# Kernel optimization log

Hardware: AMD Instinct MI355X
Metric: run time of the kernel (lower is better)

## Reference

```python
import jax, jax.numpy as jnp
import numpy as np
import math

H = 2048
NH = 16
NKV = 4
HD = H // NH  # 128
N_REP = NH // NKV
EPS = 1e-6


def rms_norm(x, w, eps=1e-6):
    x32 = x.astype(jnp.float32)
    y = x32 * jax.lax.rsqrt(jnp.mean(x32 * x32, axis=-1, keepdims=True) + eps)
    return (y * w.astype(jnp.float32)).astype(x.dtype)


def mha(normed, key_in, val_in, q_w, k_w, v_w, o_w, bias):
    # normed: [b,s,H]; key_in/val_in: [b,n,H]; bias broadcastable to [b,nh,s,n]
    b, s, _ = normed.shape
    n = key_in.shape[1]
    q = (normed @ q_w).reshape(b, s, NH, HD).transpose(0, 2, 1, 3)      # [b,nh,s,d]
    k = (key_in @ k_w).reshape(b, n, NKV, HD).transpose(0, 2, 1, 3)     # [b,nkv,n,d]
    v = (val_in @ v_w).reshape(b, n, NKV, HD).transpose(0, 2, 1, 3)
    k = jnp.repeat(k, N_REP, axis=1)  # GQA expand -> [b,nh,n,d]
    v = jnp.repeat(v, N_REP, axis=1)
    scores = jnp.einsum('bhsd,bhnd->bhsn', q, k) / math.sqrt(HD) + bias
    probs = jax.nn.softmax(scores.astype(jnp.float32), axis=-1).astype(q.dtype)
    out = jnp.einsum('bhsn,bhnd->bhsd', probs, v)
    out = out.transpose(0, 2, 1, 3).reshape(b, s, NH * HD) @ o_w
    return out, probs


def setup_inputs() -> dict:
    key = jax.random.key(0)
    ks = jax.random.split(key, 20)
    B, S, ND, T = 2, 2048, 64, 2048
    w = lambda k, sh: (jax.random.normal(k, sh, dtype=jnp.float32) * 0.02)
    return {
        'hidden_states': jax.random.normal(ks[0], (B, S, H), dtype=jnp.float32),
        'doc_summary_key': jax.random.normal(ks[1], (B, ND, H), dtype=jnp.float32),
        'doc_summary_value': jax.random.normal(ks[2], (B, ND, H), dtype=jnp.float32),
        'doc_summary_mask': jnp.ones((B, ND), dtype=jnp.float32),
        'token_key': jax.random.normal(ks[3], (B, T, H), dtype=jnp.float32),
        'token_value': jax.random.normal(ks[4], (B, T, H), dtype=jnp.float32),
        'token_mask': jnp.ones((B, T), dtype=jnp.float32),
        'cn_w': jnp.ones((H,), dtype=jnp.float32),
        'cq_w': w(ks[5], (H, NH * HD)),
        'ck_w': w(ks[6], (H, NKV * HD)),
        'cv_w': w(ks[7], (H, NKV * HD)),
        'co_w': w(ks[8], (NH * HD, H)),
        'c_gate': jnp.array([-1.0], dtype=jnp.float32),
        'fn_w': jnp.ones((H,), dtype=jnp.float32),
        'fq_w': w(ks[9], (H, NH * HD)),
        'fk_w': w(ks[10], (H, NKV * HD)),
        'fv_w': w(ks[11], (H, NKV * HD)),
        'fo_w': w(ks[12], (NH * HD, H)),
        'f_gate': jnp.array([-1.0], dtype=jnp.float32),
        'doc_token_map': jax.random.randint(ks[13], (B, T), 0, ND, dtype=jnp.int64)
            if jax.config.jax_enable_x64 else jax.random.randint(ks[13], (B, T), 0, ND).astype(jnp.int32),
    }


def reference(hidden_states, doc_summary_key, doc_summary_value, doc_summary_mask,
              token_key, token_value, token_mask,
              cn_w, cq_w, ck_w, cv_w, co_w, c_gate,
              fn_w, fq_w, fk_w, fv_w, fo_w, f_gate,
              doc_token_map):
    # ---- coarse stage: cross-attention over document summaries ----
    normed = rms_norm(hidden_states, cn_w)
    coarse_bias = ((1.0 - doc_summary_mask) * -1e9)[:, None, None, :]  # [b,1,1,nd]
    attn_out, probs = mha(normed, doc_summary_key, doc_summary_value,
                          cq_w, ck_w, cv_w, co_w, coarse_bias)
    doc_scores = probs.mean(axis=(1, 2))  # [b,nd] avg over heads+query positions
    gate_c = jax.nn.sigmoid(c_gate).astype(attn_out.dtype)
    out = hidden_states + gate_c * attn_out

    # ---- fine stage: cross-attention over token KV with log-doc-score bias ----
    log_ds = jnp.log(doc_scores + EPS)
    doc_bias = jnp.take_along_axis(log_ds, doc_token_map, axis=1)  # [b,T]
    pad_bias = (1.0 - token_mask) * -1e9
    fine_bias = (doc_bias + pad_bias)[:, None, None, :]  # [b,1,1,T]
    normed_f = rms_norm(out, fn_w)
    attn_out_f, _ = mha(normed_f, token_key, token_value,
                        fq_w, fk_w, fv_w, fo_w, fine_bias)
    gate_f = jax.nn.sigmoid(f_gate).astype(attn_out_f.dtype)
    final = out + gate_f * attn_out_f
    return final
```

## Files before the change

kernel.cpp:

```cpp
#include <hip/hip_runtime.h>
#include <hip/hip_bf16.h>

typedef unsigned short u16;
typedef unsigned int u32;
typedef __attribute__((ext_vector_type(8))) short bf16x8;
typedef __attribute__((ext_vector_type(4))) float f32x4;

constexpr int NH = 16;
constexpr int H = 2048;
constexpr float SCALE = 0.08838834764831845f;
constexpr float L2E = 1.4426950408889634f;
constexpr float SCALE2 = SCALE * L2E;
constexpr float THR2 = 8.0f * L2E;

__device__ __forceinline__ u16 f2bf(float f) {
    u32 u = __float_as_uint(f);
    u32 r = u + 0x7fffu + ((u >> 16) & 1u);
    return (u16)(r >> 16);
}
__device__ __forceinline__ u32 pack2(float x, float y) {
    return (u32)f2bf(x) | ((u32)f2bf(y) << 16);
}
__device__ __forceinline__ u32 pack2_cvt(float x, float y) {
    __hip_bfloat162 h = __float22bfloat162_rn(float2{x, y});
    return *reinterpret_cast<u32*>(&h);
}

#define GLD_LDS16(gsrc, ldst)                                                  \
    __builtin_amdgcn_global_load_lds(                                          \
        (const __attribute__((address_space(1))) void*)(gsrc),                 \
        (__attribute__((address_space(3))) void*)(ldst), 16, 0, 0)

__global__ __launch_bounds__(256) void cvt_f32_bf16(const float* __restrict__ in,
                                                    u16* __restrict__ out, int n4) {
    int i = blockIdx.x * 256 + threadIdx.x;
    if (i >= n4) return;
    float4 v = reinterpret_cast<const float4*>(in)[i];
    uint2 o;
    o.x = pack2(v.x, v.y);
    o.y = pack2(v.z, v.w);
    reinterpret_cast<uint2*>(out)[i] = o;
}

__global__ __launch_bounds__(256)
void transpose_cvt(const float* __restrict__ in, u16* __restrict__ out, int K, int N) {
    __shared__ u16 tile[32][33];
    int bn = blockIdx.x * 32, bk = blockIdx.y * 32;
    int tx = threadIdx.x & 31, ty = threadIdx.x >> 5;
#pragma unroll
    for (int r = 0; r < 32; r += 8)
        tile[tx][r + ty] = f2bf(in[(size_t)(bk + r + ty) * N + bn + tx]);
    __syncthreads();
#pragma unroll
    for (int r = 0; r < 32; r += 8)
        out[(size_t)(bn + r + ty) * K + bk + tx] = tile[r + ty][tx];
}

__global__ __launch_bounds__(256) void rmsnorm_kernel(const float* __restrict__ x,
                                                      const float* __restrict__ w,
                                                      u16* __restrict__ y) {
    int r = blockIdx.x;
    const float4* xr = reinterpret_cast<const float4*>(x + (size_t)r * H);
    int t = threadIdx.x;
    float4 v0 = xr[t * 2], v1 = xr[t * 2 + 1];
    float ss = v0.x * v0.x + v0.y * v0.y + v0.z * v0.z + v0.w * v0.w
             + v1.x * v1.x + v1.y * v1.y + v1.z * v1.z + v1.w * v1.w;
#pragma unroll
    for (int d = 1; d < 64; d <<= 1) ss += __shfl_xor(ss, d);
    __shared__ float red[4];
    if ((t & 63) == 0) red[t >> 6] = ss;
    __syncthreads();
    float tot = red[0] + red[1] + red[2] + red[3];
    float rs = rsqrtf(tot * (1.0f / H) + 1e-6f);
    const float4* wr = reinterpret_cast<const float4*>(w);
    float4 w0 = wr[t * 2], w1 = wr[t * 2 + 1];
    uint4 o;
    o.x = pack2(v0.x * rs * w0.x, v0.y * rs * w0.y);
    o.y = pack2(v0.z * rs * w0.z, v0.w * rs * w0.w);
    o.z = pack2(v1.x * rs * w1.x, v1.y * rs * w1.y);
    o.w = pack2(v1.z * rs * w1.z, v1.w * rs * w1.w);
    reinterpret_cast<uint4*>(y + (size_t)r * H)[t] = o;
}

template <int MODE, int BN>
__global__ __launch_bounds__(256)
void gemm_tn(const u16* __restrict__ A, const u16* __restrict__ Bt,
             u16* __restrict__ Cb, float* __restrict__ Cf,
             const float* __restrict__ resid, const float* __restrict__ gate_p,
             int M, int N, int K) {
    constexpr int WN = BN / 32;
    constexpr int BWROWS = BN / 4;
    __shared__ u16 As[2][128 * 64];
    __shared__ u16 Bs[2][BN * 64];
    const int t = threadIdx.x;
    const int lane = t & 63, wid = t >> 6;
    const int wm = wid >> 1, wn = wid & 1;
    const int brow = blockIdx.y * 128, bcol = blockIdx.x * BN;
    const int l15 = lane & 15, hi = lane >> 4;
    const int rsw = l15 & 7;

    f32x4 acc[4][WN] = {};
    const int srow = lane >> 3;
    const int sseg = ((lane & 7) ^ srow) * 8;
    const u16* aBase = A + (size_t)(brow + wid * 32 + srow) * K + sseg;
    const u16* bBase = Bt + (size_t)(bcol + wid * BWROWS + srow) * K + sseg;

#define GSTAGE(KT, BF)                                                          \
    do {                                                                        \
        _Pragma("unroll")                                                       \
        for (int u = 0; u < 4; ++u)                                             \
            GLD_LDS16(aBase + (size_t)(u * 8) * K + (KT),                       \
                      &As[BF][(wid * 32 + u * 8) * 64]);                        \
        _Pragma("unroll")                                                       \
        for (int u = 0; u < BWROWS / 8; ++u)                                    \
            GLD_LDS16(bBase + (size_t)(u * 8) * K + (KT),                       \
                      &Bs[BF][(wid * BWROWS + u * 8) * 64]);                    \
    } while (0)

    GSTAGE(0, 0);
    __syncthreads();
    int buf = 0;
    for (int kt = 0; kt < K; kt += 64) {
        if (kt + 64 < K) GSTAGE(kt + 64, buf ^ 1);
        bf16x8 af[4][2], bfr[WN][2];
#pragma unroll
        for (int i = 0; i < 4; ++i) {
            int row = wm * 64 + i * 16 + l15;
#pragma unroll
            for (int ko = 0; ko < 2; ++ko)
                af[i][ko] = *reinterpret_cast<const bf16x8*>(
                    &As[buf][row * 64 + (((ko * 4 + hi) ^ rsw) * 8)]);
        }
#pragma unroll
        for (int j = 0; j < WN; ++j) {
            int row = wn * (BN / 2) + j * 16 + l15;
#pragma unroll
            for (int ko = 0; ko < 2; ++ko)
                bfr[j][ko] = *reinterpret_cast<const bf16x8*>(
                    &Bs[buf][row * 64 + (((ko * 4 + hi) ^ rsw) * 8)]);
        }
#pragma unroll
        for (int ko = 0; ko < 2; ++ko)
#pragma unroll
            for (int i = 0; i < 4; ++i)
#pragma unroll
                for (int j = 0; j < WN; ++j)
                    acc[i][j] = __builtin_amdgcn_mfma_f32_16x16x32_bf16(
                        af[i][ko], bfr[j][ko], acc[i][j], 0, 0, 0);
        __syncthreads();
        buf ^= 1;
    }
#undef GSTAGE

    float g = 0.f;
    if (MODE == 1) g = 1.0f / (1.0f + expf(-gate_p[0]));
    const int r0 = hi * 4, c0 = l15;
#pragma unroll
    for (int i = 0; i < 4; ++i) {
#pragma unroll
        for (int j = 0; j < WN; ++j) {
            int col = bcol + wn * (BN / 2) + j * 16 + c0;
#pragma unroll
            for (int r = 0; r < 4; ++r) {
                int row = brow + wm * 64 + i * 16 + r0 + r;
                float v = acc[i][j][r];
                if (MODE == 0) Cb[(size_t)row * N + col] = f2bf(v);
                else Cf[(size_t)row * N + col] = resid[(size_t)row * N + col] + g * v;
            }
        }
    }
}

__global__ __launch_bounds__(256)
void coarse_attn(const u16* __restrict__ q, const u16* __restrict__ kc,
                 const u16* __restrict__ vc, const float* __restrict__ mask,
                 float* __restrict__ doc_part, u16* __restrict__ attn_c) {
    constexpr int SC = 2048 / 64;
    int bid = blockIdx.x;
    int b = bid / (NH * SC);
    int rem = bid % (NH * SC);
    int h = rem / SC, sc = rem % SC;
    int kv = h >> 2;
    int t = threadIdx.x, lane = t & 63, wid = t >> 6;
    const int l15 = lane & 15, k0 = (lane >> 4) * 8;

    __shared__ u16 Kt[64 * 136];
    __shared__ u16 Vt[128 * 72];
    __shared__ u16 Pt[4][16 * 72];
    __shared__ float p_acc[64];

    {
        int n = t >> 2, s2 = t & 3;
        const u16* src = kc + (size_t)(b * 64 + n) * 512 + kv * 128;
#pragma unroll
        for (int u = 0; u < 4; ++u) {
            int sg = s2 + u * 4;
            *reinterpret_cast<uint4*>(&Kt[n * 136 + sg * 8]) =
                *reinterpret_cast<const uint4*>(src + sg * 8);
        }
    }
    {
        int n = t & 63, dblk = t >> 6;
        const u16* src = vc + (size_t)(b * 64 + n) * 512 + kv * 128 + dblk * 32;
#pragma unroll
        for (int u = 0; u < 4; ++u) {
            u16 tmp[8];
            *reinterpret_cast<uint4*>(tmp) = *reinterpret_cast<const uint4*>(src + u * 8);
#pragma unroll
            for (int e = 0; e < 8; ++e) Vt[(dblk * 32 + u * 8 + e) * 72 + n] = tmp[e];
        }
    }
    if (t < 64) p_acc[t] = 0.f;
    __syncthreads();

    int qrow = sc * 64 + wid * 16 + l15;
    const u16* qsrc = q + (size_t)(b * 2048 + qrow) * 2048 + h * 128;
    bf16x8 af[4];
#pragma unroll
    for (int kk = 0; kk < 4; ++kk)
        af[kk] = *reinterpret_cast<const bf16x8*>(qsrc + kk * 32 + k0);

    f32x4 sc4[4] = {};
#pragma unroll
    for (int kk = 0; kk < 4; ++kk)
#pragma unroll
        for (int j = 0; j < 4; ++j) {
            bf16x8 bfr = *reinterpret_cast<const bf16x8*>(&Kt[(j * 16 + l15) * 136 + kk * 32 + k0]);
            sc4[j] = __builtin_amdgcn_mfma_f32_16x16x32_bf16(af[kk], bfr, sc4[j], 0, 0, 0);
        }

    float s[4][4];
#pragma unroll
    for (int j = 0; j < 4; ++j) {
        float bia = (1.0f - mask[b * 64 + j * 16 + l15]) * (-1e9f * L2E);
#pragma unroll
        for (int r = 0; r < 4; ++r) s[j][r] = sc4[j][r] * SCALE2 + bia;
    }
    float m4[4], l4[4];
#pragma unroll
    for (int r = 0; r < 4; ++r) {
        float m = fmaxf(fmaxf(s[0][r], s[1][r]), fmaxf(s[2][r], s[3][r]));
#pragma unroll
        for (int d = 1; d < 16; d <<= 1) m = fmaxf(m, __shfl_xor(m, d));
        m4[r] = m;
    }
#pragma unroll
    for (int r = 0; r < 4; ++r) {
        float l = 0.f;
#pragma unroll
        for (int j = 0; j < 4; ++j) { s[j][r] = exp2f(s[j][r] - m4[r]); l += s[j][r]; }
#pragma unroll
        for (int d = 1; d < 16; d <<= 1) l += __shfl_xor(l, d);
        l4[r] = l;
    }
#pragma unroll
    for (int j = 0; j < 4; ++j) {
        float cs = 0.f;
#pragma unroll
        for (int r = 0; r < 4; ++r) {
            float pr = s[j][r] / l4[r];
            Pt[wid][((lane >> 4) * 4 + r) * 72 + j * 16 + l15] = f2bf(pr);
            cs += pr;
        }
        cs += __shfl_xor(cs, 16);
        cs += __shfl_xor(cs, 32);
        if (lane < 16) atomicAdd(&p_acc[j * 16 + lane], cs);
    }
    __syncthreads();

    f32x4 o4[8] = {};
#pragma unroll
    for (int kk2 = 0; kk2 < 2; ++kk2) {
        bf16x8 a2 = *reinterpret_cast<const bf16x8*>(&Pt[wid][l15 * 72 + kk2 * 32 + k0]);
#pragma unroll
        for (int j2 = 0; j2 < 8; ++j2) {
            bf16x8 b2 = *reinterpret_cast<const bf16x8*>(&Vt[(j2 * 16 + l15) * 72 + kk2 * 32 + k0]);
            o4[j2] = __builtin_amdgcn_mfma_f32_16x16x32_bf16(a2, b2, o4[j2], 0, 0, 0);
        }
    }
#pragma unroll
    for (int j2 = 0; j2 < 8; ++j2)
#pragma unroll
        for (int r = 0; r < 4; ++r) {
            int row = sc * 64 + wid * 16 + (lane >> 4) * 4 + r;
            attn_c[(size_t)(b * 2048 + row) * 2048 + h * 128 + j2 * 16 + l15] = f2bf(o4[j2][r]);
        }
    if (t < 64) atomicAdd(&doc_part[(blockIdx.x & 7) * 128 + b * 64 + t], p_acc[t]);
}

__global__ void doc_finalize(const float* __restrict__ doc_part, float* __restrict__ log_ds) {
    int t = threadIdx.x;
    float s = 0.f;
#pragma unroll
    for (int i = 0; i < 8; ++i) s += doc_part[i * 128 + t];
    log_ds[t] = logf(s / 32768.0f + 1e-6f);
}

__global__ __launch_bounds__(256)
void bias_kernel(const float* __restrict__ log_ds, const int* __restrict__ map,
                 const float* __restrict__ tmask, float* __restrict__ bias) {
    int i = blockIdx.x * 256 + threadIdx.x;
    if (i >= 2 * 2048) return;
    int b = i >> 11;
    bias[i] = (log_ds[b * 64 + map[i]] + (1.0f - tmask[i]) * -1e9f) * L2E;
}

__global__ __launch_bounds__(256, 2)
void flash_attn(const u16* __restrict__ q, const u16* __restrict__ kf,
                const u16* __restrict__ vT, const float* __restrict__ bias,
                u16* __restrict__ attn_f) {
    int bid = blockIdx.x;
    int b = bid >> 8;
    int rem = bid & 255;
    int h = rem >> 4, sc = rem & 15;
    int kv = h >> 2;
    int t = threadIdx.x, lane = t & 63, wid = t >> 6;
    const int l15 = lane & 15, hi = lane >> 4;
    const int k0 = hi * 8;
    const int rswp = l15 & 7;

    __shared__ u16 Kt[2][64 * 128];
    __shared__ u16 Vt[128 * 64];
    __shared__ u16 Pt[4][32 * 64];

    bf16x8 qf4[2][4];
#pragma unroll
    for (int f = 0; f < 2; ++f) {
        int qrow = sc * 128 + wid * 32 + f * 16 + l15;
        const u16* qsrc = q + (size_t)(b * 2048 + qrow) * 2048 + h * 128;
#pragma unroll
        for (int kk = 0; kk < 4; ++kk)
            qf4[f][kk] = *reinterpret_cast<const bf16x8*>(qsrc + kk * 32 + k0);
    }

    const int krl = lane >> 4, kslot = lane & 15;
    const int vrl = lane >> 3, vslot = lane & 7;
    const u16* kbase = kf + (size_t)(b * 2048) * 512 + kv * 128;
    const u16* vbase = vT + (size_t)(kv * 128) * 4096 + b * 2048;
    const float* bbase = bias + b * 2048;

#define STAGE_K(TT, BF)                                                            \
    do {                                                                           \
        _Pragma("unroll")                                                          \
        for (int u = 0; u < 4; ++u) {                                              \
            int row = wid * 16 + u * 4 + krl;                                      \
            const u16* src = kbase + (size_t)((TT) + row) * 512                    \
                             + ((kslot ^ (row & 7)) * 8);                          \
            GLD_LDS16(src, &Kt[BF][(wid * 16 + u * 4) * 128]);                     \
        }                                                                          \
    } while (0)
#define STAGE_V(TT)                                                                \
    do {                                                                           \
        _Pragma("unroll")                                                          \
        for (int u = 0; u < 4; ++u) {                                              \
            int row = wid * 32 + u * 8 + vrl;                                      \
            const u16* src = vbase + (size_t)row * 4096 + (TT)                     \
                             + ((vslot ^ (row & 7)) * 8);                          \
            GLD_LDS16(src, &Vt[(wid * 32 + u * 8) * 64]);                          \
        }                                                                          \
    } while (0)

    float mstate[2] = {-1e30f, -1e30f}, lstate[2] = {0.f, 0.f};
    f32x4 o4[2][8] = {};

    STAGE_K(0, 0);
    __syncthreads();
    int kbuf = 0;

    for (int t0 = 0; t0 < 2048; t0 += 64) {
        int t1 = (t0 + 64) & 2047;
        STAGE_K(t1, kbuf ^ 1);
        STAGE_V(t0);

        f32x4 st0[4] = {}, st1[4] = {};
        __builtin_amdgcn_s_setprio(1);
#pragma unroll
        for (int kk = 0; kk < 4; ++kk)
#pragma unroll
            for (int kb = 0; kb < 4; ++kb) {
                int row = kb * 16 + l15;
                bf16x8 kfrag = *reinterpret_cast<const bf16x8*>(
                    &Kt[kbuf][row * 128 + (((kk * 4 + hi) ^ (row & 7)) * 8)]);
                st0[kb] = __builtin_amdgcn_mfma_f32_16x16x32_bf16(kfrag, qf4[0][kk], st0[kb], 0, 0, 0);
                st1[kb] = __builtin_amdgcn_mfma_f32_16x16x32_bf16(kfrag, qf4[1][kk], st1[kb], 0, 0, 0);
            }
        __builtin_amdgcn_s_setprio(0);

        float p[2][4][4];
        float pmax[2] = {-1e30f, -1e30f};
#pragma unroll
        for (int kb = 0; kb < 4; ++kb) {
            float4 b4 = *reinterpret_cast<const float4*>(bbase + t0 + kb * 16 + hi * 4);
            float bb[4] = {b4.x, b4.y, b4.z, b4.w};
#pragma unroll
            for (int r = 0; r < 4; ++r) {
                float v0 = st0[kb][r] * SCALE2 + bb[r];
                float v1 = st1[kb][r] * SCALE2 + bb[r];
                p[0][kb][r] = v0;
                p[1][kb][r] = v1;
                pmax[0] = fmaxf(pmax[0], v0);
                pmax[1] = fmaxf(pmax[1], v1);
            }
        }
#pragma unroll
        for (int f = 0; f < 2; ++f) {
            pmax[f] = fmaxf(pmax[f], __shfl_xor(pmax[f], 16));
            pmax[f] = fmaxf(pmax[f], __shfl_xor(pmax[f], 32));
        }

        bool need = (pmax[0] > mstate[0] + THR2) || (pmax[1] > mstate[1] + THR2);
        if (__any(need)) {
#pragma unroll
            for (int f = 0; f < 2; ++f) {
                float mnew = fmaxf(mstate[f], pmax[f]);
                float sco = exp2f(mstate[f] - mnew);
                float sco_out[4];
#pragma unroll
                for (int r = 0; r < 4; ++r) sco_out[r] = __shfl(sco, hi * 4 + r);
#pragma unroll
                for (int j2 = 0; j2 < 8; ++j2)
#pragma unroll
                    for (int r = 0; r < 4; ++r) o4[f][j2][r] *= sco_out[r];
                lstate[f] *= sco;
                mstate[f] = mnew;
            }
        }

#pragma unroll
        for (int f = 0; f < 2; ++f) {
            float lt = 0.f;
#pragma unroll
            for (int kb = 0; kb < 4; ++kb)
#pragma unroll
                for (int r = 0; r < 4; ++r) {
                    p[f][kb][r] = exp2f(p[f][kb][r] - mstate[f]);
                    lt += p[f][kb][r];
                }
            lt += __shfl_xor(lt, 16);
            lt += __shfl_xor(lt, 32);
            lstate[f] += lt;
        }

#pragma unroll
        for (int f = 0; f < 2; ++f)
#pragma unroll
            for (int kb = 0; kb < 4; ++kb) {
                uint2 w;
                w.x = pack2_cvt(p[f][kb][0], p[f][kb][1]);
                w.y = pack2_cvt(p[f][kb][2], p[f][kb][3]);
                int idx = (f * 16 + l15) * 64
                        + (((kb * 2 + (hi >> 1)) ^ rswp) * 8) + (hi & 1) * 4;
                *reinterpret_cast<uint2*>(&Pt[wid][idx]) = w;
            }

        __syncthreads();

        __builtin_amdgcn_s_setprio(1);
#pragma unroll
        for (int kc = 0; kc < 2; ++kc) {
            bf16x8 pa0 = *reinterpret_cast<const bf16x8*>(
                &Pt[wid][l15 * 64 + (((kc * 4 + hi) ^ rswp) * 8)]);
            bf16x8 pa1 = *reinterpret_cast<const bf16x8*>(
                &Pt[wid][(16 + l15) * 64 + (((kc * 4 + hi) ^ rswp) * 8)]);
#pragma unroll
            for (int j2 = 0; j2 < 8; ++j2) {
                int d = j2 * 16 + l15;
                bf16x8 vb = *reinterpret_cast<const bf16x8*>(
                    &Vt[d * 64 + (((kc * 4 + hi) ^ (d & 7)) * 8)]);
                o4[0][j2] = __builtin_amdgcn_mfma_f32_16x16x32_bf16(pa0, vb, o4[0][j2], 0, 0, 0);
                o4[1][j2] = __builtin_amdgcn_mfma_f32_16x16x32_bf16(pa1, vb, o4[1][j2], 0, 0, 0);
            }
        }
        __builtin_amdgcn_s_setprio(0);
        __syncthreads();
        kbuf ^= 1;
    }
#undef STAGE_K
#undef STAGE_V

#pragma unroll
    for (int f = 0; f < 2; ++f) {
        float linv[4];
#pragma unroll
        for (int r = 0; r < 4; ++r) linv[r] = 1.0f / __shfl(lstate[f], hi * 4 + r);
#pragma unroll
        for (int j2 = 0; j2 < 8; ++j2)
#pragma unroll
            for (int r = 0; r < 4; ++r) {
                int row = sc * 128 + wid * 32 + f * 16 + hi * 4 + r;
                attn_f[(size_t)(b * 2048 + row) * 2048 + h * 128 + j2 * 16 + l15] =
                    f2bf(o4[f][j2][r] * linv[r]);
            }
    }
}

extern "C" void kernel_launch(void* const* d_in, const int* in_sizes, int n_in,
                              void* d_out, int out_size, void* d_ws, size_t ws_size,
                              hipStream_t stream) {
    const float* hidden = (const float*)d_in[0];
    const float* dsk    = (const float*)d_in[1];
    const float* dsv    = (const float*)d_in[2];
    const float* dsmask = (const float*)d_in[3];
    const float* tk     = (const float*)d_in[4];
    const float* tv     = (const float*)d_in[5];
    const float* tmask  = (const float*)d_in[6];
    const float* cn_w   = (const float*)d_in[7];
    const float* cq_w   = (const float*)d_in[8];
    const float* ck_w   = (const float*)d_in[9];
    const float* cv_w   = (const float*)d_in[10];
    const float* co_w   = (const float*)d_in[11];
    const float* c_gate = (const float*)d_in[12];
    const float* fn_w   = (const float*)d_in[13];
    const float* fq_w   = (const float*)d_in[14];
    const float* fk_w   = (const float*)d_in[15];
    const float* fv_w   = (const float*)d_in[16];
    const float* fo_w   = (const float*)d_in[17];
    const float* f_gate = (const float*)d_in[18];
    const int*   map    = (const int*)d_in[19];
    float* out_f = (float*)d_out;

    char* ws = (char*)d_ws;
    size_t off = 0;
    auto alloc = [&](size_t bytes) {
        char* p = ws + off;
        off += (bytes + 255) & ~(size_t)255;
        return p;
    };
    u16*  normA = (u16*)alloc(4096ULL * 2048 * 2);
    u16*  qbuf  = (u16*)alloc(4096ULL * 2048 * 2);
    u16*  kc    = (u16*)alloc(128ULL * 512 * 2);
    u16*  vc    = (u16*)alloc(128ULL * 512 * 2);
    u16*  dskb  = (u16*)alloc(128ULL * 2048 * 2);
    u16*  dsvb  = (u16*)alloc(128ULL * 2048 * 2);
    u16*  kfb   = (u16*)alloc(4096ULL * 512 * 2);
    u16*  vTb   = (u16*)alloc(512ULL * 4096 * 2);
    u16*  cqT   = (u16*)alloc(2048ULL * 2048 * 2);
    u16*  ckT   = (u16*)alloc(512ULL * 2048 * 2);
    u16*  cvT   = (u16*)alloc(512ULL * 2048 * 2);
    u16*  coT   = (u16*)alloc(2048ULL * 2048 * 2);
    u16*  fqT   = (u16*)alloc(2048ULL * 2048 * 2);
    u16*  fkT   = (u16*)alloc(512ULL * 2048 * 2);
    u16*  fvT   = (u16*)alloc(512ULL * 2048 * 2);
    u16*  foT   = (u16*)alloc(2048ULL * 2048 * 2);
    float* doc_part = (float*)alloc(8 * 128 * 4);
    float* log_ds   = (float*)alloc(128 * 4);
    float* biasb    = (float*)alloc(4096 * 4);

    hipMemsetAsync(doc_part, 0, 8 * 128 * 4, stream);

    transpose_cvt<<<dim3(64, 64), 256, 0, stream>>>(cq_w, cqT, 2048, 2048);
    transpose_cvt<<<dim3(16, 64), 256, 0, stream>>>(ck_w, ckT, 2048, 512);
    transpose_cvt<<<dim3(16, 64), 256, 0, stream>>>(cv_w, cvT, 2048, 512);
    transpose_cvt<<<dim3(64, 64), 256, 0, stream>>>(co_w, coT, 2048, 2048);
    transpose_cvt<<<dim3(64, 64), 256, 0, stream>>>(fq_w, fqT, 2048, 2048);
    transpose_cvt<<<dim3(16, 64), 256, 0, stream>>>(fk_w, fkT, 2048, 512);
    transpose_cvt<<<dim3(16, 64), 256, 0, stream>>>(fv_w, fvT, 2048, 512);
    transpose_cvt<<<dim3(64, 64), 256, 0, stream>>>(fo_w, foT, 2048, 2048);

    cvt_f32_bf16<<<(128 * 2048 / 4 + 255) / 256, 256, 0, stream>>>(dsk, dskb, 128 * 2048 / 4);
    cvt_f32_bf16<<<(128 * 2048 / 4 + 255) / 256, 256, 0, stream>>>(dsv, dsvb, 128 * 2048 / 4);
    rmsnorm_kernel<<<4096, 256, 0, stream>>>(hidden, cn_w, normA);

    gemm_tn<0, 128><<<dim3(16, 32), 256, 0, stream>>>(normA, cqT, qbuf, nullptr, nullptr, nullptr, 4096, 2048, 2048);
    gemm_tn<0, 64><<<dim3(8, 1), 256, 0, stream>>>(dskb, ckT, kc, nullptr, nullptr, nullptr, 128, 512, 2048);
    gemm_tn<0, 64><<<dim3(8, 1), 256, 0, stream>>>(dsvb, cvT, vc, nullptr, nullptr, nullptr, 128, 512, 2048);

    coarse_attn<<<1024, 256, 0, stream>>>(qbuf, kc, vc, dsmask, doc_part, normA);
    doc_finalize<<<1, 128, 0, stream>>>(doc_part, log_ds);
    bias_kernel<<<16, 256, 0, stream>>>(log_ds, map, tmask, biasb);

    gemm_tn<1, 128><<<dim3(16, 32), 256, 0, stream>>>(normA, coT, nullptr, out_f, hidden, c_gate, 4096, 2048, 2048);

    rmsnorm_kernel<<<4096, 256, 0, stream>>>(out_f, fn_w, qbuf);
    gemm_tn<0, 128><<<dim3(16, 32), 256, 0, stream>>>(qbuf, fqT, normA, nullptr, nullptr, nullptr, 4096, 2048, 2048);
    cvt_f32_bf16<<<(4096 * 2048 / 4 + 255) / 256, 256, 0, stream>>>(tk, qbuf, 4096 * 2048 / 4);
    gemm_tn<0, 64><<<dim3(8, 32), 256, 0, stream>>>(qbuf, fkT, kfb, nullptr, nullptr, nullptr, 4096, 512, 2048);
    cvt_f32_bf16<<<(4096 * 2048 / 4 + 255) / 256, 256, 0, stream>>>(tv, qbuf, 4096 * 2048 / 4);
    gemm_tn<0, 64><<<dim3(64, 4), 256, 0, stream>>>(fvT, qbuf, vTb, nullptr, nullptr, nullptr, 512, 4096, 2048);

    flash_attn<<<512, 256, 0, stream>>>(normA, kfb, vTb, biasb, qbuf);

    gemm_tn<1, 128><<<dim3(16, 32), 256, 0, stream>>>(qbuf, foT, nullptr, out_f, out_f, f_gate, 4096, 2048, 2048);
}
```

Baseline: 499.9 us.

## Batch small launches, swizzle GEMM block order, double-buffer V in flash attention

Merges the eight weight transpose launches into two batched launches, merges the two conversion launches and the two small K/V GEMMs into z-indexed kernels, and folds doc_finalize into bias_kernel. The intent is to cut kernel launch overhead. GEMM workgroups are remapped with an XCD-aware swizzle so that neighbouring tiles land on the same die for L2 reuse. Flash attention now double-buffers V alongside K and drops one __syncthreads per iteration, which overlaps loads with compute at the cost of extra LDS and possibly lower occupancy.

```diff
diff --git a/kernel.cpp b/kernel.cpp
--- a/kernel.cpp
+++ b/kernel.cpp
@@ -30,6 +30,23 @@
     __builtin_amdgcn_global_load_lds(                                          \
         (const __attribute__((address_space(1))) void*)(gsrc),                 \
         (__attribute__((address_space(3))) void*)(ldst), 16, 0, 0)
+
+__global__ __launch_bounds__(256) void cvt_f32_bf16_2(const float* __restrict__ a,
+                                                      u16* __restrict__ oa,
+                                                      const float* __restrict__ b,
+                                                      u16* __restrict__ ob, int n4) {
+    int i = blockIdx.x * 256 + threadIdx.x;
+    const float* in;
+    u16* out;
+    if (i < n4) { in = a; out = oa; }
+    else if (i < 2 * n4) { i -= n4; in = b; out = ob; }
+    else return;
+    float4 v = reinterpret_cast<const float4*>(in)[i];
+    uint2 o;
+    o.x = pack2(v.x, v.y);
+    o.y = pack2(v.z, v.w);
+    reinterpret_cast<uint2*>(out)[i] = o;
+}
 
 __global__ __launch_bounds__(256) void cvt_f32_bf16(const float* __restrict__ in,
                                                     u16* __restrict__ out, int n4) {
@@ -43,7 +60,14 @@
 }
 
 __global__ __launch_bounds__(256)
-void transpose_cvt(const float* __restrict__ in, u16* __restrict__ out, int K, int N) {
+void transpose_cvt4(const float* __restrict__ i0, const float* __restrict__ i1,
+                    const float* __restrict__ i2, const float* __restrict__ i3,
+                    u16* __restrict__ o0, u16* __restrict__ o1,
+                    u16* __restrict__ o2, u16* __restrict__ o3, int K, int N) {
+    const float* in = (blockIdx.z == 0) ? i0 : (blockIdx.z == 1) ? i1
+                    : (blockIdx.z == 2) ? i2 : i3;
+    u16* out = (blockIdx.z == 0) ? o0 : (blockIdx.z == 1) ? o1
+             : (blockIdx.z == 2) ? o2 : o3;
     __shared__ u16 tile[32][33];
     int bn = blockIdx.x * 32, bk = blockIdx.y * 32;
     int tx = threadIdx.x & 31, ty = threadIdx.x >> 5;
@@ -83,11 +107,11 @@
 }
 
 template <int MODE, int BN>
-__global__ __launch_bounds__(256)
-void gemm_tn(const u16* __restrict__ A, const u16* __restrict__ Bt,
-             u16* __restrict__ Cb, float* __restrict__ Cf,
-             const float* __restrict__ resid, const float* __restrict__ gate_p,
-             int M, int N, int K) {
+__device__ __forceinline__
+void gemm_body(const u16* __restrict__ A, const u16* __restrict__ Bt,
+               u16* __restrict__ Cb, float* __restrict__ Cf,
+               const float* __restrict__ resid, const float* __restrict__ gate_p,
+               int N, int K, int brow, int bcol) {
     constexpr int WN = BN / 32;
     constexpr int BWROWS = BN / 4;
     __shared__ u16 As[2][128 * 64];
@@ -95,7 +119,6 @@
     const int t = threadIdx.x;
     const int lane = t & 63, wid = t >> 6;
     const int wm = wid >> 1, wn = wid & 1;
-    const int brow = blockIdx.y * 128, bcol = blockIdx.x * BN;
     const int l15 = lane & 15, hi = lane >> 4;
     const int rsw = l15 & 7;
 
@@ -169,6 +192,32 @@
             }
         }
     }
+}
+
+template <int MODE, int BN>
+__global__ __launch_bounds__(256)
+void gemm_tn(const u16* __restrict__ A, const u16* __restrict__ Bt,
+             u16* __restrict__ Cb, float* __restrict__ Cf,
+             const float* __restrict__ resid, const float* __restrict__ gate_p,
+             int M, int N, int K) {
+    int nbx = gridDim.x;
+    int nwg = nbx * gridDim.y;
+    int lin = blockIdx.y * nbx + blockIdx.x;
+    if (!(nwg & 7)) { int q = nwg >> 3; lin = (lin & 7) * q + (lin >> 3); }
+    gemm_body<MODE, BN>(A, Bt, Cb, Cf, resid, gate_p, N, K,
+                        (lin / nbx) * 128, (lin % nbx) * BN);
+}
+
+template <int MODE, int BN>
+__global__ __launch_bounds__(256)
+void gemm_tn_z2(const u16* __restrict__ A0, const u16* __restrict__ B0, u16* __restrict__ C0,
+                const u16* __restrict__ A1, const u16* __restrict__ B1, u16* __restrict__ C1,
+                int N, int K) {
+    const u16* A = blockIdx.z ? A1 : A0;
+    const u16* B = blockIdx.z ? B1 : B0;
+    u16* C = blockIdx.z ? C1 : C0;
+    gemm_body<MODE, BN>(A, B, C, nullptr, nullptr, nullptr, N, K,
+                        blockIdx.y * 128, blockIdx.x * BN);
 }
 
 __global__ __launch_bounds__(256)
@@ -288,21 +337,22 @@
     if (t < 64) atomicAdd(&doc_part[(blockIdx.x & 7) * 128 + b * 64 + t], p_acc[t]);
 }
 
-__global__ void doc_finalize(const float* __restrict__ doc_part, float* __restrict__ log_ds) {
+__global__ __launch_bounds__(256)
+void bias_kernel(const float* __restrict__ doc_part, const int* __restrict__ map,
+                 const float* __restrict__ tmask, float* __restrict__ bias) {
+    __shared__ float lg[128];
     int t = threadIdx.x;
-    float s = 0.f;
-#pragma unroll
-    for (int i = 0; i < 8; ++i) s += doc_part[i * 128 + t];
-    log_ds[t] = logf(s / 32768.0f + 1e-6f);
-}
-
-__global__ __launch_bounds__(256)
-void bias_kernel(const float* __restrict__ log_ds, const int* __restrict__ map,
-                 const float* __restrict__ tmask, float* __restrict__ bias) {
-    int i = blockIdx.x * 256 + threadIdx.x;
+    if (t < 128) {
+        float s = 0.f;
+#pragma unroll
+        for (int i = 0; i < 8; ++i) s += doc_part[i * 128 + t];
+        lg[t] = logf(s / 32768.0f + 1e-6f);
+    }
+    __syncthreads();
+    int i = blockIdx.x * 256 + t;
     if (i >= 2 * 2048) return;
     int b = i >> 11;
-    bias[i] = (log_ds[b * 64 + map[i]] + (1.0f - tmask[i]) * -1e9f) * L2E;
+    bias[i] = (lg[b * 64 + map[i]] + (1.0f - tmask[i]) * -1e9f) * L2E;
 }
 
 __global__ __launch_bounds__(256, 2)
@@ -320,7 +370,7 @@
     const int rswp = l15 & 7;
 
     __shared__ u16 Kt[2][64 * 128];
-    __shared__ u16 Vt[128 * 64];
+    __shared__ u16 Vt[2][128 * 64];
     __shared__ u16 Pt[4][32 * 64];
 
     bf16x8 qf4[2][4];
@@ -349,14 +399,14 @@
             GLD_LDS16(src, &Kt[BF][(wid * 16 + u * 4) * 128]);                     \
         }                                                                          \
     } while (0)
-#define STAGE_V(TT)                                                                \
+#define STAGE_V(TT, BF)                                                            \
     do {                                                                           \
         _Pragma("unroll")                                                          \
         for (int u = 0; u < 4; ++u) {                                              \
             int row = wid * 32 + u * 8 + vrl;                                      \
             const u16* src = vbase + (size_t)row * 4096 + (TT)                     \
                              + ((vslot ^ (row & 7)) * 8);                          \
-            GLD_LDS16(src, &Vt[(wid * 32 + u * 8) * 64]);                          \
+            GLD_LDS16(src, &Vt[BF][(wid * 32 + u * 8) * 64]);                      \
         }                                                                          \
     } while (0)
 
@@ -364,13 +414,14 @@
     f32x4 o4[2][8] = {};
 
     STAGE_K(0, 0);
+    STAGE_V(0, 0);
     __syncthreads();
-    int kbuf = 0;
+    int par = 0;
 
     for (int t0 = 0; t0 < 2048; t0 += 64) {
         int t1 = (t0 + 64) & 2047;
-        STAGE_K(t1, kbuf ^ 1);
-        STAGE_V(t0);
+        STAGE_K(t1, par ^ 1);
+        STAGE_V(t1, par ^ 1);
 
         f32x4 st0[4] = {}, st1[4] = {};
         __builtin_amdgcn_s_setprio(1);
@@ -380,7 +431,7 @@
             for (int kb = 0; kb < 4; ++kb) {
                 int row = kb * 16 + l15;
                 bf16x8 kfrag = *reinterpret_cast<const bf16x8*>(
-                    &Kt[kbuf][row * 128 + (((kk * 4 + hi) ^ (row & 7)) * 8)]);
+                    &Kt[par][row * 128 + (((kk * 4 + hi) ^ (row & 7)) * 8)]);
                 st0[kb] = __builtin_amdgcn_mfma_f32_16x16x32_bf16(kfrag, qf4[0][kk], st0[kb], 0, 0, 0);
                 st1[kb] = __builtin_amdgcn_mfma_f32_16x16x32_bf16(kfrag, qf4[1][kk], st1[kb], 0, 0, 0);
             }
@@ -453,8 +504,6 @@
                 *reinterpret_cast<uint2*>(&Pt[wid][idx]) = w;
             }
 
-        __syncthreads();
-
         __builtin_amdgcn_s_setprio(1);
 #pragma unroll
         for (int kc = 0; kc < 2; ++kc) {
@@ -466,14 +515,14 @@
             for (int j2 = 0; j2 < 8; ++j2) {
                 int d = j2 * 16 + l15;
                 bf16x8 vb = *reinterpret_cast<const bf16x8*>(
-                    &Vt[d * 64 + (((kc * 4 + hi) ^ (d & 7)) * 8)]);
+                    &Vt[par][d * 64 + (((kc * 4 + hi) ^ (d & 7)) * 8)]);
                 o4[0][j2] = __builtin_amdgcn_mfma_f32_16x16x32_bf16(pa0, vb, o4[0][j2], 0, 0, 0);
                 o4[1][j2] = __builtin_amdgcn_mfma_f32_16x16x32_bf16(pa1, vb, o4[1][j2], 0, 0, 0);
             }
         }
         __builtin_amdgcn_s_setprio(0);
         __syncthreads();
-        kbuf ^= 1;
+        par ^= 1;
     }
 #undef STAGE_K
 #undef STAGE_V
@@ -543,31 +592,24 @@
     u16*  fvT   = (u16*)alloc(512ULL * 2048 * 2);
     u16*  foT   = (u16*)alloc(2048ULL * 2048 * 2);
     float* doc_part = (float*)alloc(8 * 128 * 4);
-    float* log_ds   = (float*)alloc(128 * 4);
     float* biasb    = (float*)alloc(4096 * 4);
 
     hipMemsetAsync(doc_part, 0, 8 * 128 * 4, stream);
 
-    transpose_cvt<<<dim3(64, 64), 256, 0, stream>>>(cq_w, cqT, 2048, 2048);
-    transpose_cvt<<<dim3(16, 64), 256, 0, stream>>>(ck_w, ckT, 2048, 512);
-    transpose_cvt<<<dim3(16, 64), 256, 0, stream>>>(cv_w, cvT, 2048, 512);
-    transpose_cvt<<<dim3(64, 64), 256, 0, stream>>>(co_w, coT, 2048, 2048);
-    transpose_cvt<<<dim3(64, 64), 256, 0, stream>>>(fq_w, fqT, 2048, 2048);
-    transpose_cvt<<<dim3(16, 64), 256, 0, stream>>>(fk_w, fkT, 2048, 512);
-    transpose_cvt<<<dim3(16, 64), 256, 0, stream>>>(fv_w, fvT, 2048, 512);
-    transpose_cvt<<<dim3(64, 64), 256, 0, stream>>>(fo_w, foT, 2048, 2048);
-
-    cvt_f32_bf16<<<(128 * 2048 / 4 + 255) / 256, 256, 0, stream>>>(dsk, dskb, 128 * 2048 / 4);
-    cvt_f32_bf16<<<(128 * 2048 / 4 + 255) / 256, 256, 0, stream>>>(dsv, dsvb, 128 * 2048 / 4);
+    transpose_cvt4<<<dim3(64, 64, 4), 256, 0, stream>>>(cq_w, co_w, fq_w, fo_w,
+                                                        cqT, coT, fqT, foT, 2048, 2048);
+    transpose_cvt4<<<dim3(16, 64, 4), 256, 0, stream>>>(ck_w, cv_w, fk_w, fv_w,
+                                                        ckT, cvT, fkT, fvT, 2048, 512);
+
+    cvt_f32_bf16_2<<<(2 * 128 * 2048 / 4 + 255) / 256, 256, 0, stream>>>(
+        dsk, dskb, dsv, dsvb, 128 * 2048 / 4);
     rmsnorm_kernel<<<4096, 256, 0, stream>>>(hidden, cn_w, normA);
 
     gemm_tn<0, 128><<<dim3(16, 32), 256, 0, stream>>>(normA, cqT, qbuf, nullptr, nullptr, nullptr, 4096, 2048, 2048);
-    gemm_tn<0, 64><<<dim3(8, 1), 256, 0, stream>>>(dskb, ckT, kc, nullptr, nullptr, nullptr, 128, 512, 2048);
-    gemm_tn<0, 64><<<dim3(8, 1), 256, 0, stream>>>(dsvb, cvT, vc, nullptr, nullptr, nullptr, 128, 512, 2048);
+    gemm_tn_z2<0, 64><<<dim3(8, 1, 2), 256, 0, stream>>>(dskb, ckT, kc, dsvb, cvT, vc, 512, 2048);
 
     coarse_attn<<<1024, 256, 0, stream>>>(qbuf, kc, vc, dsmask, doc_part, normA);
-    doc_finalize<<<1, 128, 0, stream>>>(doc_part, log_ds);
-    bias_kernel<<<16, 256, 0, stream>>>(log_ds, map, tmask, biasb);
+    bias_kernel<<<16, 256, 0, stream>>>(doc_part, map, tmask, biasb);
 
     gemm_tn<1, 128><<<dim3(16, 32), 256, 0, stream>>>(normA, coT, nullptr, out_f, hidden, c_gate, 4096, 2048, 2048);
 
```

New measurement: 448.9 us. 10.2% less time.
